# Kernel optimization log

Hardware: AMD Instinct MI355X
Metric: run time of the kernel (lower is better)

The kernel has to match this reference:

```python
import jax, jax.numpy as jnp
import numpy as np

ALPHA = 1.0
NUM_GROUPS = 4  # groups take values in {0,1,2,3}


def setup_inputs() -> dict:
    key = jax.random.key(0)
    k1, k2 = jax.random.split(key)
    B, C = 2000000, 14
    inputs = jax.random.normal(k1, (B, C), dtype=jnp.float32)
    targets = jax.random.randint(k2, (B, C), 0, 2).astype(jnp.float32)
    # fixed group assignment per label (init arg `groups`)
    groups = jnp.array([0, 1, 1, 2, 2, 0, 3, 3, 1, 2, 0, 3, 1, 2], dtype=jnp.int32)
    return {"inputs": inputs, "targets": targets, "groups": groups}


def reference(inputs, targets, groups):
    x, t = inputs, targets
    # BCE with logits, no pos_weight: max(x,0) - x*t + log(1 + exp(-|x|))
    bce = jnp.maximum(x, 0.0) - x * t + jnp.log1p(jnp.exp(-jnp.abs(x)))  # [B, C]
    # per-sample sum of targets within each group: [NUM_GROUPS, B]
    group_sums = jax.ops.segment_sum(t.T, groups, num_segments=NUM_GROUPS)
    # gather each label's group sum back: [C, B]
    gathered = group_sums[groups]
    # group 0 is always kept; other groups kept only if their target sum > 0
    mask = jnp.where(groups[:, None] == 0, 1.0, (gathered > 0).astype(bce.dtype))  # [C, B]
    loss = bce * mask.T * ALPHA  # [B, C]
    return jnp.mean(loss)
```

## Files before the change

### kernel.cpp

```cpp
#include <hip/hip_runtime.h>

#define NCH 14
#define BT 256
#define LN2F 0.69314718055994530942f

#define EXPECTED_PACK ((0u<<0)|(1u<<2)|(1u<<4)|(2u<<6)|(2u<<8)|(0u<<10)|(3u<<12)|(3u<<14)| \
                       (1u<<16)|(2u<<18)|(0u<<20)|(3u<<22)|(1u<<24)|(2u<<26))

__device__ __forceinline__ unsigned make_pack(const int* __restrict__ groups) {
    unsigned p = 0u;
#pragma unroll
    for (int c = 0; c < NCH; ++c) p |= ((unsigned)(groups[c] & 3)) << (2 * c);
    return p;
}

__device__ __forceinline__ void row_spec(const float* xs, const float* ts,
                                         float& accL, float& accG) {
    float lin[NCH], lg[NCH];
#pragma unroll
    for (int c = 0; c < NCH; ++c) {
        float xv = xs[c];
        lin[c] = fmaf(-xv, ts[c], fmaxf(xv, 0.0f));
        float z = __expf(-fabsf(xv));
        lg[c] = __log2f(1.0f + z);
    }
    float s1 = ts[1] + ts[2] + ts[8] + ts[12];
    float s2 = ts[3] + ts[4] + ts[9] + ts[13];
    float s3 = ts[6] + ts[7] + ts[11];

    float rL0 = lin[0] + lin[5] + lin[10],            rG0 = lg[0] + lg[5] + lg[10];
    float rL1 = lin[1] + lin[2] + lin[8] + lin[12],   rG1 = lg[1] + lg[2] + lg[8] + lg[12];
    float rL2 = lin[3] + lin[4] + lin[9] + lin[13],   rG2 = lg[3] + lg[4] + lg[9] + lg[13];
    float rL3 = lin[6] + lin[7] + lin[11],            rG3 = lg[6] + lg[7] + lg[11];

    accL += rL0;                        accG += rG0;
    accL += (s1 > 0.0f) ? rL1 : 0.0f;   accG += (s1 > 0.0f) ? rG1 : 0.0f;
    accL += (s2 > 0.0f) ? rL2 : 0.0f;   accG += (s2 > 0.0f) ? rG2 : 0.0f;
    accL += (s3 > 0.0f) ? rL3 : 0.0f;   accG += (s3 > 0.0f) ? rG3 : 0.0f;
}

__device__ __forceinline__ void row_gen(const float* xs, const float* ts,
                                        unsigned pack, float& accL, float& accG) {
    unsigned gb = 0u;
#pragma unroll
    for (int c = 0; c < NCH; ++c) {
        int gc = (pack >> (2 * c)) & 3;
        gb |= (ts[c] > 0.0f) ? (1u << gc) : 0u;
    }
#pragma unroll
    for (int c = 0; c < NCH; ++c) {
        int gc = (pack >> (2 * c)) & 3;
        float xv = xs[c];
        float lin = fmaf(-xv, ts[c], fmaxf(xv, 0.0f));
        float lg = __log2f(1.0f + __expf(-fabsf(xv)));
        bool keep = (gc == 0) || ((gb >> gc) & 1u);
        accL += keep ? lin : 0.0f;
        accG += keep ? lg : 0.0f;
    }
}

__global__ __launch_bounds__(BT) void bce_partial(
    const float* __restrict__ x, const float* __restrict__ t,
    const int* __restrict__ groups, float* __restrict__ partial,
    int rows, int iters)
{
    const unsigned pack = make_pack(groups);
    const bool spec = (pack == EXPECTED_PACK);
    const int pairs = rows >> 1;
    const int nth = gridDim.x * BT;

    float accL = 0.0f, accG = 0.0f;

    for (int it = 0; it < iters; ++it) {
        const int p = blockIdx.x * BT + threadIdx.x + it * nth;
        if (p < pairs) {
            const float4* xp = (const float4*)(x + (size_t)p * (2 * NCH));
            const float4* tp = (const float4*)(t + (size_t)p * (2 * NCH));
            float xs[2 * NCH], ts[2 * NCH];
#pragma unroll
            for (int j = 0; j < 7; ++j) {
                float4 a = xp[j];
                float4 b = tp[j];
                xs[4 * j + 0] = a.x; xs[4 * j + 1] = a.y; xs[4 * j + 2] = a.z; xs[4 * j + 3] = a.w;
                ts[4 * j + 0] = b.x; ts[4 * j + 1] = b.y; ts[4 * j + 2] = b.z; ts[4 * j + 3] = b.w;
            }
            if (spec) {
                row_spec(xs, ts, accL, accG);
                row_spec(xs + NCH, ts + NCH, accL, accG);
            } else {
                row_gen(xs, ts, pack, accL, accG);
                row_gen(xs + NCH, ts + NCH, pack, accL, accG);
            }
        }
    }

    if ((rows & 1) && blockIdx.x == 0 && threadIdx.x == 0) {
        const size_t base = (size_t)(rows - 1) * NCH;
        float xs[NCH], ts[NCH];
#pragma unroll
        for (int c = 0; c < NCH; ++c) { xs[c] = x[base + c]; ts[c] = t[base + c]; }
        row_gen(xs, ts, pack, accL, accG);
    }

    float acc = fmaf(LN2F, accG, accL);

#pragma unroll
    for (int off = 32; off > 0; off >>= 1) acc += __shfl_xor(acc, off);

    __shared__ float wsum[BT / 64];
    const int lane = threadIdx.x & 63;
    const int wid = threadIdx.x >> 6;
    if (lane == 0) wsum[wid] = acc;
    __syncthreads();
    if (threadIdx.x == 0)
        partial[blockIdx.x] = wsum[0] + wsum[1] + wsum[2] + wsum[3];
}

__global__ __launch_bounds__(256) void finalize(
    const float* __restrict__ partial, int n, float* __restrict__ out, double inv_count)
{
    double s = 0.0;
    for (int i = threadIdx.x; i < n; i += 256) s += (double)partial[i];

    __shared__ double sd[256];
    sd[threadIdx.x] = s;
    __syncthreads();
#pragma unroll
    for (int step = 128; step > 0; step >>= 1) {
        if (threadIdx.x < step) sd[threadIdx.x] += sd[threadIdx.x + step];
        __syncthreads();
    }
    if (threadIdx.x == 0) out[0] = (float)(sd[0] * inv_count);
}

extern "C" void kernel_launch(void* const* d_in, const int* in_sizes, int n_in,
                              void* d_out, int out_size, void* d_ws, size_t ws_size,
                              hipStream_t stream) {
    const float* x = (const float*)d_in[0];
    const float* t = (const float*)d_in[1];
    const int* groups = (const int*)d_in[2];
    float* out = (float*)d_out;
    float* partial = (float*)d_ws;

    const int total = in_sizes[0];
    const int rows = total / NCH;
    const int pairs = rows >> 1;

    int blocks = (pairs + BT - 1) / BT;
    if ((size_t)blocks * sizeof(float) > ws_size)
        blocks = (int)(ws_size / sizeof(float));
    if (blocks < 1) blocks = 1;
    const int iters = (pairs + blocks * BT - 1) / (blocks * BT);

    bce_partial<<<blocks, BT, 0, stream>>>(x, t, groups, partial, rows, iters);

    const double inv_count = 1.0 / ((double)rows * (double)NCH);
    finalize<<<1, 256, 0, stream>>>(partial, blocks, out, inv_count);
}
```

Baseline: 44.94 us.

## Use a fixed persistent grid with double-buffered register prefetch of row pairs

The one-pair-per-thread launch is replaced by a fixed 512-block grid-stride loop, and each thread keeps two register buffers. It loads the next pair while computing the current one, so memory latency overlaps with the transcendental math. The launch bound is raised to request two blocks per SM. The cost is much higher register pressure from the 56 float4 buffers, which could reduce occupancy or cause spills, and 512 blocks may underfill the 256-CU device's latency hiding.

```diff
diff --git a/kernel.cpp b/kernel.cpp
--- a/kernel.cpp
+++ b/kernel.cpp
@@ -2,6 +2,7 @@
 
 #define NCH 14
 #define BT 256
+#define NBLOCKS 512
 #define LN2F 0.69314718055994530942f
 
 #define EXPECTED_PACK ((0u<<0)|(1u<<2)|(1u<<4)|(2u<<6)|(2u<<8)|(0u<<10)|(3u<<12)|(3u<<14)| \
@@ -21,8 +22,7 @@
     for (int c = 0; c < NCH; ++c) {
         float xv = xs[c];
         lin[c] = fmaf(-xv, ts[c], fmaxf(xv, 0.0f));
-        float z = __expf(-fabsf(xv));
-        lg[c] = __log2f(1.0f + z);
+        lg[c] = __log2f(1.0f + __expf(-fabsf(xv)));
     }
     float s1 = ts[1] + ts[2] + ts[8] + ts[12];
     float s2 = ts[3] + ts[4] + ts[9] + ts[13];
@@ -59,7 +59,34 @@
     }
 }
 
-__global__ __launch_bounds__(BT) void bce_partial(
+__device__ __forceinline__ void compute_pair(const float4* xv, const float4* tv,
+                                             bool spec, unsigned pack,
+                                             float& accL, float& accG) {
+    float xs[2 * NCH], ts[2 * NCH];
+#pragma unroll
+    for (int j = 0; j < 7; ++j) {
+        xs[4 * j + 0] = xv[j].x; xs[4 * j + 1] = xv[j].y;
+        xs[4 * j + 2] = xv[j].z; xs[4 * j + 3] = xv[j].w;
+        ts[4 * j + 0] = tv[j].x; ts[4 * j + 1] = tv[j].y;
+        ts[4 * j + 2] = tv[j].z; ts[4 * j + 3] = tv[j].w;
+    }
+    if (spec) {
+        row_spec(xs, ts, accL, accG);
+        row_spec(xs + NCH, ts + NCH, accL, accG);
+    } else {
+        row_gen(xs, ts, pack, accL, accG);
+        row_gen(xs + NCH, ts + NCH, pack, accL, accG);
+    }
+}
+
+#define LOADP(XR, TRR, pp) do {                                        \
+    const float4* xp_ = (const float4*)(x + (size_t)(pp) * (2 * NCH)); \
+    const float4* tp_ = (const float4*)(t + (size_t)(pp) * (2 * NCH)); \
+    _Pragma("unroll")                                                  \
+    for (int j_ = 0; j_ < 7; ++j_) { XR[j_] = xp_[j_]; TRR[j_] = tp_[j_]; } \
+} while (0)
+
+__global__ __launch_bounds__(BT, 2) void bce_partial(
     const float* __restrict__ x, const float* __restrict__ t,
     const int* __restrict__ groups, float* __restrict__ partial,
     int rows, int iters)
@@ -67,31 +94,24 @@
     const unsigned pack = make_pack(groups);
     const bool spec = (pack == EXPECTED_PACK);
     const int pairs = rows >> 1;
-    const int nth = gridDim.x * BT;
+    const int stride = gridDim.x * BT;
 
     float accL = 0.0f, accG = 0.0f;
 
-    for (int it = 0; it < iters; ++it) {
-        const int p = blockIdx.x * BT + threadIdx.x + it * nth;
-        if (p < pairs) {
-            const float4* xp = (const float4*)(x + (size_t)p * (2 * NCH));
-            const float4* tp = (const float4*)(t + (size_t)p * (2 * NCH));
-            float xs[2 * NCH], ts[2 * NCH];
-#pragma unroll
-            for (int j = 0; j < 7; ++j) {
-                float4 a = xp[j];
-                float4 b = tp[j];
-                xs[4 * j + 0] = a.x; xs[4 * j + 1] = a.y; xs[4 * j + 2] = a.z; xs[4 * j + 3] = a.w;
-                ts[4 * j + 0] = b.x; ts[4 * j + 1] = b.y; ts[4 * j + 2] = b.z; ts[4 * j + 3] = b.w;
-            }
-            if (spec) {
-                row_spec(xs, ts, accL, accG);
-                row_spec(xs + NCH, ts + NCH, accL, accG);
-            } else {
-                row_gen(xs, ts, pack, accL, accG);
-                row_gen(xs + NCH, ts + NCH, pack, accL, accG);
-            }
-        }
+    float4 xa[7], ta[7], xb[7], tb[7];
+    int p = blockIdx.x * BT + threadIdx.x;
+    if (p < pairs) LOADP(xa, ta, p);
+
+    for (int it = 0; it < iters; it += 2) {
+        const int p1 = p + stride;
+        if ((it + 1) < iters && p1 < pairs) LOADP(xb, tb, p1);
+        if (p < pairs) compute_pair(xa, ta, spec, pack, accL, accG);
+
+        const int p2 = p1 + stride;
+        if ((it + 2) < iters && p2 < pairs) LOADP(xa, ta, p2);
+        if ((it + 1) < iters && p1 < pairs) compute_pair(xb, tb, spec, pack, accL, accG);
+
+        p = p2;
     }
 
     if ((rows & 1) && blockIdx.x == 0 && threadIdx.x == 0) {
@@ -146,7 +166,9 @@
     const int rows = total / NCH;
     const int pairs = rows >> 1;
 
-    int blocks = (pairs + BT - 1) / BT;
+    int blocks = NBLOCKS;
+    const int maxb = (pairs + BT - 1) / BT;
+    if (blocks > maxb) blocks = maxb;
     if ((size_t)blocks * sizeof(float) > ws_size)
         blocks = (int)(ws_size / sizeof(float));
     if (blocks < 1) blocks = 1;
```

Measured after the change: 42.99 us. 1.05x faster.
